# Kernel tuning notes

Measured on AMD Instinct MI355X. Metric: run time of the kernel, lower is better.

## Reference

```python
import jax, jax.numpy as jnp
import numpy as np

IGNORE_INDEX = 0


def _lovasz_softmax(inputs, targets):
    # inputs: [B, C, H, W] logits; targets: [B, H, W] int class ids
    C = inputs.shape[1]
    probs = jax.nn.softmax(inputs, axis=1)                      # [B,C,H,W]
    probs_flat = probs.transpose(0, 2, 3, 1).reshape(-1, C)     # [P,C]
    t = targets.reshape(-1)                                     # [P]
    valid = (t != IGNORE_INDEX)                                 # [P] bool

    # Per-class foreground indicator, zeroed at invalid pixels: [C,P]
    fg = ((t[None, :] == jnp.arange(C)[:, None]) & valid[None, :]).astype(probs_flat.dtype)
    # Errors |fg - prob|; invalid pixels forced to error 0 so they sort to the
    # end and contribute nothing (equivalent to filtering them out, since both
    # their error and the causal cumsums at earlier positions are unaffected).
    errors = jnp.abs(fg - probs_flat.T) * valid[None, :].astype(probs_flat.dtype)  # [C,P]

    # Sort each class's errors descending; permutation is non-differentiable (constant).
    order = jnp.argsort(-errors, axis=1)                        # [C,P]
    errors_sorted = jnp.take_along_axis(errors, order, axis=1)
    fg_sorted = jnp.take_along_axis(fg, order, axis=1)

    # Lovasz gradient (Alg. 1), vectorized over classes.
    gts = fg_sorted.sum(axis=1, keepdims=True)                  # [C,1]
    intersection = gts - jnp.cumsum(fg_sorted, axis=1)
    union = gts + jnp.cumsum(1.0 - fg_sorted, axis=1)
    jaccard = 1.0 - intersection / union                        # [C,P]
    grad = jnp.concatenate([jaccard[:, :1], jaccard[:, 1:] - jaccard[:, :-1]], axis=1)

    per_class = jnp.sum(jax.nn.relu(errors_sorted) * jax.lax.stop_gradient(grad), axis=1)  # [C]

    # classes='present': only classes with foreground among valid pixels, skip ignore_index.
    present = (fg.sum(axis=1) > 0) & (jnp.arange(C) != IGNORE_INDEX)  # [C] bool
    n_present = jnp.sum(present.astype(per_class.dtype))
    total = jnp.sum(jnp.where(present, per_class, 0.0))
    return jnp.where(n_present > 0, total / jnp.maximum(n_present, 1.0), 0.0)


def setup_inputs() -> dict:
    key = jax.random.key(0)
    k1, k2 = jax.random.split(key)
    B, C, H, W = 8, 8, 512, 512
    inputs = jax.random.normal(k1, (B, C, H, W), dtype=jnp.float32)
    targets = jax.random.randint(k2, (B, H, W), 0, C, dtype=jnp.int32)
    return {"inputs": inputs, "targets": targets}


def reference(inputs, targets):
    return _lovasz_softmax(inputs, targets)
```

## Files before the change

kernel.cpp:

```cpp
#include <hip/hip_runtime.h>
#include <stdint.h>

#define HW      262144
#define NCLASS  8
#define PIX     2097152
#define NCLS    7
#define KB      512
#define BLOCK   1024
#define CHUNK   4096
#define NBLK    (PIX / CHUNK)
#define NCOPY   8
#define HSZ     (NCLS * KB)
#define ZERO_BYTES (NCOPY * HSZ * 8)

__global__ __launch_bounds__(BLOCK) void lovasz_hist_kernel(
    const float* __restrict__ logits, const int* __restrict__ targets,
    unsigned long long* __restrict__ gNF)
{
    __shared__ unsigned int sPacked[HSZ];

    const int tid = threadIdx.x;
    for (int i = tid; i < HSZ; i += BLOCK) sPacked[i] = 0u;
    __syncthreads();

    const int p0 = blockIdx.x * CHUNK + tid * 4;
    const int b  = p0 >> 18;
    const int hw = p0 & (HW - 1);
    const float* xp = logits + (size_t)b * (NCLASS * HW) + hw;

    const int4 t4 = *(const int4*)(targets + p0);
    float4 x4[NCLASS];
    #pragma unroll
    for (int c = 0; c < NCLASS; ++c)
        x4[c] = *(const float4*)(xp + (size_t)c * HW);

    const int tarr[4] = {t4.x, t4.y, t4.z, t4.w};
    #pragma unroll
    for (int j = 0; j < 4; ++j) {
        const int t = tarr[j];
        if (t == 0) continue;
        float x[NCLASS];
        #pragma unroll
        for (int c = 0; c < NCLASS; ++c)
            x[c] = (j == 0) ? x4[c].x : (j == 1) ? x4[c].y
                 : (j == 2) ? x4[c].z : x4[c].w;

        float m = x[0];
        #pragma unroll
        for (int c = 1; c < NCLASS; ++c) m = fmaxf(m, x[c]);
        float s = 0.0f;
        float ex[NCLASS];
        #pragma unroll
        for (int c = 0; c < NCLASS; ++c) { ex[c] = __expf(x[c] - m); s += ex[c]; }
        const float inv = 1.0f / s;
        #pragma unroll
        for (int c = 1; c < NCLASS; ++c) {
            const float pc = ex[c] * inv;
            const bool  fg = (t == c);
            const float err = fg ? (1.0f - pc) : pc;
            int k = (int)(err * (float)KB);
            k = (k > KB - 1) ? (KB - 1) : k;
            atomicAdd(&sPacked[(c - 1) * KB + k], fg ? 0x10001u : 1u);
        }
    }
    __syncthreads();

    unsigned long long* g = gNF + (size_t)(blockIdx.x & (NCOPY - 1)) * HSZ;
    for (int i = tid; i < HSZ; i += BLOCK) {
        const unsigned pk = sPacked[i];
        if (pk) {
            const unsigned long long v =
                ((unsigned long long)(pk >> 16) << 32) | (unsigned long long)(pk & 0xFFFFu);
            atomicAdd(&g[i], v);
        }
    }
}

__global__ __launch_bounds__(NCLS * 64) void lovasz_scan_kernel(
    const unsigned long long* __restrict__ gNF, float* __restrict__ out)
{
    const int wid  = threadIdx.x >> 6;
    const int lane = threadIdx.x & 63;

    unsigned int n[8], f[8];
    unsigned long long tnf = 0ull;
    #pragma unroll
    for (int j = 0; j < 8; ++j) {
        const int k = KB - 1 - (lane * 8 + j);
        unsigned long long v = 0ull;
        #pragma unroll
        for (int r = 0; r < NCOPY; ++r)
            v += gNF[(size_t)r * HSZ + wid * KB + k];
        n[j] = (unsigned)(v & 0xFFFFFFFFull);
        f[j] = (unsigned)(v >> 32);
        tnf += (unsigned long long)n[j] | ((unsigned long long)f[j] << 32);
    }

    unsigned long long inc = tnf;
    #pragma unroll
    for (int off = 1; off < 64; off <<= 1) {
        const unsigned long long u = __shfl_up(inc, off, 64);
        if (lane >= off) inc += u;
    }
    const unsigned long long tot = __shfl(inc, 63, 64);
    const unsigned int G = (unsigned)(tot >> 32);

    double contrib = 0.0;
    if (G > 0) {
        const unsigned long long exc = inc - tnf;
        long long i0 = (long long)(unsigned)(exc & 0xFFFFFFFFull);
        long long F0 = (long long)(unsigned)(exc >> 32);
        const long long Gl = (long long)G;
        #pragma unroll
        for (int j = 0; j < 8; ++j) {
            if (n[j]) {
                const long long i1 = i0 + n[j];
                const long long F1 = F0 + f[j];
                const long long num = (Gl - F0) * (Gl + i1 - F1)
                                    - (Gl - F1) * (Gl + i0 - F0);
                const double den = (double)(Gl + i0 - F0) * (double)(Gl + i1 - F1);
                const double dJ = (double)num / den;
                const double e = ((double)(KB - 1 - (lane * 8 + j)) + 0.5) / (double)KB;
                contrib += e * dJ;
            }
            i0 += n[j]; F0 += f[j];
        }
    }

    #pragma unroll
    for (int off = 32; off > 0; off >>= 1)
        contrib += __shfl_down(contrib, off, 64);

    __shared__ double sSum[NCLS];
    __shared__ int    sCnt[NCLS];
    if (lane == 0) { sSum[wid] = contrib; sCnt[wid] = (G > 0) ? 1 : 0; }
    __syncthreads();
    if (threadIdx.x == 0) {
        double s = 0.0; int cnt = 0;
        #pragma unroll
        for (int c = 0; c < NCLS; ++c) { s += sSum[c]; cnt += sCnt[c]; }
        out[0] = (cnt > 0) ? (float)(s / (double)cnt) : 0.0f;
    }
}

extern "C" void kernel_launch(void* const* d_in, const int* in_sizes, int n_in,
                              void* d_out, int out_size, void* d_ws, size_t ws_size,
                              hipStream_t stream) {
    const float* logits  = (const float*)d_in[0];
    const int*   targets = (const int*)d_in[1];
    float* out = (float*)d_out;
    unsigned long long* gNF = (unsigned long long*)d_ws;

    hipMemsetAsync(d_ws, 0, ZERO_BYTES, stream);
    lovasz_hist_kernel<<<NBLK, BLOCK, 0, stream>>>(logits, targets, gNF);
    lovasz_scan_kernel<<<1, NCLS * 64, 0, stream>>>(gNF, out);
}
```

Measured before the change: 110.8 us.

## Split histogram: 4 classes in LDS, 3 classes via global atomics with 32 copies

The change keeps LDS histograms for classes 1-4 only. Classes 5-7 go straight to global 64-bit atomics spread over 32 copies, chosen by lane XOR block index, so that LDS atomic contention is spread across two memory paths. The scan kernel now reduces the two regions separately, and the softmax divide uses a fast hardware reciprocal. The cost is about two million global atomic operations hitting L2, plus a larger memset of the workspace.

Result: slower. 409.1 us (+269.4%).

```diff
diff --git a/kernel.cpp b/kernel.cpp
--- a/kernel.cpp
+++ b/kernel.cpp
@@ -9,19 +9,31 @@
 #define BLOCK   1024
 #define CHUNK   4096
 #define NBLK    (PIX / CHUNK)
-#define NCOPY   8
 #define HSZ     (NCLS * KB)
-#define ZERO_BYTES (NCOPY * HSZ * 8)
+
+#define ROWS_A  4
+#define NCOPY_A 8
+#define ROWS_B  3
+#define NCOPY_B 32
+#define STR_B   (ROWS_B * KB)
+#define WORDS_A (NCOPY_A * HSZ)
+#define WORDS_B (NCOPY_B * STR_B)
+#define ZERO_BYTES ((WORDS_A + WORDS_B) * 8)
 
 __global__ __launch_bounds__(BLOCK) void lovasz_hist_kernel(
     const float* __restrict__ logits, const int* __restrict__ targets,
-    unsigned long long* __restrict__ gNF)
+    unsigned long long* __restrict__ gA)
 {
-    __shared__ unsigned int sPacked[HSZ];
+    unsigned long long* __restrict__ gB = gA + WORDS_A;
+
+    __shared__ unsigned int sPacked[ROWS_A * KB];
 
     const int tid = threadIdx.x;
-    for (int i = tid; i < HSZ; i += BLOCK) sPacked[i] = 0u;
+    for (int i = tid; i < ROWS_A * KB; i += BLOCK) sPacked[i] = 0u;
     __syncthreads();
+
+    const unsigned copyB = ((unsigned)tid & 31u) ^ ((unsigned)blockIdx.x & 31u);
+    unsigned long long* __restrict__ myB = gB + (size_t)copyB * STR_B;
 
     const int p0 = blockIdx.x * CHUNK + tid * 4;
     const int b  = p0 >> 18;
@@ -52,7 +64,7 @@
         float ex[NCLASS];
         #pragma unroll
         for (int c = 0; c < NCLASS; ++c) { ex[c] = __expf(x[c] - m); s += ex[c]; }
-        const float inv = 1.0f / s;
+        const float inv = __builtin_amdgcn_rcpf(s);
         #pragma unroll
         for (int c = 1; c < NCLASS; ++c) {
             const float pc = ex[c] * inv;
@@ -60,13 +72,18 @@
             const float err = fg ? (1.0f - pc) : pc;
             int k = (int)(err * (float)KB);
             k = (k > KB - 1) ? (KB - 1) : k;
-            atomicAdd(&sPacked[(c - 1) * KB + k], fg ? 0x10001u : 1u);
+            if (c <= ROWS_A) {
+                atomicAdd(&sPacked[(c - 1) * KB + k], fg ? 0x10001u : 1u);
+            } else {
+                atomicAdd(&myB[(c - 1 - ROWS_A) * KB + k],
+                          fg ? 0x100000001ull : 1ull);
+            }
         }
     }
     __syncthreads();
 
-    unsigned long long* g = gNF + (size_t)(blockIdx.x & (NCOPY - 1)) * HSZ;
-    for (int i = tid; i < HSZ; i += BLOCK) {
+    unsigned long long* g = gA + (size_t)(blockIdx.x & (NCOPY_A - 1)) * HSZ;
+    for (int i = tid; i < ROWS_A * KB; i += BLOCK) {
         const unsigned pk = sPacked[i];
         if (pk) {
             const unsigned long long v =
@@ -77,8 +94,9 @@
 }
 
 __global__ __launch_bounds__(NCLS * 64) void lovasz_scan_kernel(
-    const unsigned long long* __restrict__ gNF, float* __restrict__ out)
+    const unsigned long long* __restrict__ gA, float* __restrict__ out)
 {
+    const unsigned long long* __restrict__ gB = gA + WORDS_A;
     const int wid  = threadIdx.x >> 6;
     const int lane = threadIdx.x & 63;
 
@@ -88,9 +106,15 @@
     for (int j = 0; j < 8; ++j) {
         const int k = KB - 1 - (lane * 8 + j);
         unsigned long long v = 0ull;
-        #pragma unroll
-        for (int r = 0; r < NCOPY; ++r)
-            v += gNF[(size_t)r * HSZ + wid * KB + k];
+        if (wid < ROWS_A) {
+            #pragma unroll
+            for (int r = 0; r < NCOPY_A; ++r)
+                v += gA[(size_t)r * HSZ + wid * KB + k];
+        } else {
+            #pragma unroll
+            for (int r = 0; r < NCOPY_B; ++r)
+                v += gB[(size_t)r * STR_B + (wid - ROWS_A) * KB + k];
+        }
         n[j] = (unsigned)(v & 0xFFFFFFFFull);
         f[j] = (unsigned)(v >> 32);
         tnf += (unsigned long long)n[j] | ((unsigned long long)f[j] << 32);
@@ -149,9 +173,9 @@
     const float* logits  = (const float*)d_in[0];
     const int*   targets = (const int*)d_in[1];
     float* out = (float*)d_out;
-    unsigned long long* gNF = (unsigned long long*)d_ws;
+    unsigned long long* gA = (unsigned long long*)d_ws;
 
     hipMemsetAsync(d_ws, 0, ZERO_BYTES, stream);
-    lovasz_hist_kernel<<<NBLK, BLOCK, 0, stream>>>(logits, targets, gNF);
-    lovasz_scan_kernel<<<1, NCLS * 64, 0, stream>>>(gNF, out);
+    lovasz_hist_kernel<<<NBLK, BLOCK, 0, stream>>>(logits, targets, gA);
+    lovasz_scan_kernel<<<1, NCLS * 64, 0, stream>>>(gA, out);
 }
```
